# Kernel optimization log

Measured on AMD Instinct MI355X. Metric: run time of the kernel, lower is better.

## Reference

```python
import jax, jax.numpy as jnp
import numpy as np

B, N = 2, 200
IMG = 2048
NC = 4                    # node concepts ('Is*')
NODE_CH = NC * 256        # 1024
EC = 3                    # edge concepts minus 'HigherPri'
AC = 4                    # actions
BBOX_MAX = 1024.0
E = N * (N - 1)

# static fully-connected directed edge list (src=i, dst=j, i!=j), row-major order
_ii, _jj = np.meshgrid(np.arange(N), np.arange(N), indexing='ij')
_m = _ii != _jj
SRC = jnp.asarray(_ii[_m])
DST = jnp.asarray(_jj[_m])


def _lin(k, fin, fout):
    kw, kb = jax.random.split(k)
    s = 1.0 / np.sqrt(fin)
    return (jax.random.uniform(kw, (fin, fout), jnp.float32, -s, s),
            jax.random.uniform(kb, (fout,), jnp.float32, -s, s))


def setup_inputs():
    ks = jax.random.split(jax.random.key(0), 16)
    p = {}
    p['roi_features'] = jax.random.normal(ks[0], (B, N, IMG), jnp.float32)
    p['batch_bboxes'] = jax.random.uniform(ks[1], (B, N, 4), jnp.float32) * BBOX_MAX
    p['batch_directions'] = jax.random.normal(ks[2], (B, N, 4), jnp.float32)
    p['batch_priorities'] = jax.random.normal(ks[3], (B, N), jnp.float32)
    p['w1'], p['b1'] = _lin(ks[4], IMG, 512)
    p['w2'], p['b2'] = _lin(ks[5], 512, 256)
    p['w3'], p['b3'] = _lin(ks[6], 256, NODE_CH)
    p['wi'], p['bi'] = _lin(ks[7], NODE_CH, NC)
    p['we1'], p['be1'] = _lin(ks[8], 16, 256)
    p['we2'], p['be2'] = _lin(ks[9], 256, 64)
    p['we3'], p['be3'] = _lin(ks[10], 64, EC)
    p['wp1'], p['bp1'] = _lin(ks[11], EC + 1, 128)
    p['wp2'], p['bp2'] = _lin(ks[12], 128, NODE_CH * AC)
    p['root_w'], _ = _lin(ks[13], NODE_CH, AC)
    _, p['root_b'] = _lin(ks[14], NODE_CH, AC)
    return p


def reference(roi_features, batch_bboxes, batch_directions, batch_priorities,
              w1, b1, w2, b2, w3, b3, wi, bi,
              we1, be1, we2, be2, we3, be3,
              wp1, bp1, wp2, bp2, root_w, root_b):
    # node concept embedding MLP: [B,N,IMG] -> [B,N,NODE_CH]
    h = jax.nn.relu(roi_features @ w1 + b1)
    h = jax.nn.relu(h @ w2 + b2)
    node_concepts = h @ w3 + b3
    node_concepts_explicit = jax.nn.sigmoid(node_concepts @ wi + bi)

    # pairwise attributes for all directed edges (same ordering as torch masks)
    node_attr = jnp.concatenate([batch_bboxes / BBOX_MAX, batch_directions], -1)  # [B,N,8]
    pair = jnp.concatenate([node_attr[:, SRC], node_attr[:, DST]], -1)            # [B,E,16]
    eh = jax.nn.relu(pair @ we1 + be1)
    eh = jax.nn.relu(eh @ we2 + be2)
    edge_attributes = jax.nn.sigmoid(eh @ we3 + be3)                              # [B,E,EC]
    higher_pri = (batch_priorities[:, SRC] > batch_priorities[:, DST]).astype(jnp.float32)
    edge_attributes = jnp.concatenate([edge_attributes, higher_pri[..., None]], -1)  # [B,E,EC+1]

    # NNConv on graph 0: per-edge weight matrix, gather-matmul-scatter
    x = node_concepts[0]                 # [N, NODE_CH]
    e = edge_attributes[0]               # [E, EC+1]
    w = jax.nn.relu(e @ wp1 + bp1) @ wp2 + bp2
    w = w.reshape(E, NODE_CH, AC)        # [E, NODE_CH, AC]
    msg = jnp.einsum('ei,eio->eo', x[SRC], w)          # [E, AC]
    agg = jax.ops.segment_sum(msg, DST, num_segments=N)  # [N, AC]
    next_actions = agg + x @ root_w + root_b
    return (next_actions, node_concepts_explicit[0], edge_attributes[0])
```

## Files before the change

### kernel.cpp

```cpp
#include <hip/hip_runtime.h>
#include <math.h>

#define NN 200
#define ETOT 39800

typedef float float4v __attribute__((ext_vector_type(4)));
typedef short short8 __attribute__((ext_vector_type(8)));
typedef unsigned int uint4v __attribute__((ext_vector_type(4)));

__device__ __forceinline__ float sigf(float x) { return 1.0f / (1.0f + expf(-x)); }

__device__ __forceinline__ unsigned short f2b(float f) {
  unsigned u = __float_as_uint(f);
  u += 0x7fffu + ((u >> 16) & 1u);
  return (unsigned short)(u >> 16);
}
__device__ __forceinline__ float b2f16(unsigned short u) {
  return __uint_as_float(((unsigned)u) << 16);
}
__device__ __forceinline__ unsigned pkbf(float a, float b) {
  return (unsigned)f2b(a) | ((unsigned)f2b(b) << 16);
}

__global__ __launch_bounds__(256) void k_prep(
    const float* __restrict__ w1, const float* __restrict__ w2, const float* __restrict__ w3,
    const float* __restrict__ wp2, const float* __restrict__ we2,
    const float* __restrict__ bbox, const float* __restrict__ dir,
    const float* __restrict__ we1, const float* __restrict__ be1,
    const float* __restrict__ roi, const float* __restrict__ wp1,
    unsigned short* __restrict__ w1T, unsigned short* __restrict__ w2T,
    unsigned short* __restrict__ w3T, unsigned short* __restrict__ WrT,
    unsigned short* __restrict__ we2T, unsigned short* __restrict__ roiB,
    float* __restrict__ P, float* __restrict__ Q, float* __restrict__ wp1T) {
  __shared__ float lds[64][65];
  const int b = blockIdx.x, tid = threadIdx.x;

  if (b < 352) {
    const float* Wf;
    unsigned short* Wt;
    int K, N, t;
    if (b < 256) { Wf = w1; Wt = w1T; K = 2048; N = 512; t = b; }
    else if (b < 288) { Wf = w2; Wt = w2T; K = 512; N = 256; t = b - 256; }
    else { Wf = w3; Wt = w3T; K = 256; N = 1024; t = b - 288; }
    const int K64 = K >> 6;
    const int kt = t % K64, nt = t / K64;
#pragma unroll 4
    for (int i = 0; i < 16; ++i) {
      int idx = tid + i * 256;
      int r = idx >> 6, c = idx & 63;
      lds[r][c] = Wf[(size_t)(kt * 64 + r) * N + nt * 64 + c];
    }
    __syncthreads();
#pragma unroll 4
    for (int i = 0; i < 16; ++i) {
      int idx = tid + i * 256;
      int r = idx >> 6, c = idx & 63;
      Wt[(size_t)(nt * 64 + r) * K + kt * 64 + c] = f2b(lds[c][r]);
    }
  } else if (b < 480) {
    int k = b - 352;
    int o = tid >> 6, l = tid & 63;
    const float* src = wp2 + (size_t)k * 4096;
    unsigned short* dst = WrT + (size_t)(k * 4 + o) * 1024;
    for (int i = l; i < 1024; i += 64) dst[i] = f2b(src[i * 4 + o]);
  } else if (b < 496) {
    int f = (b - 480) * 256 + tid;
    int c = f >> 6, k0 = (f & 63) * 4;
#pragma unroll
    for (int q = 0; q < 4; ++q)
      we2T[c * 256 + k0 + q] = f2b(we2[(k0 + q) * 64 + c]);
  } else if (b < 696) {
    int n = b - 496, c = tid;
    float a[8];
#pragma unroll
    for (int r = 0; r < 4; ++r) a[r] = bbox[n * 4 + r] * (1.0f / 1024.0f);
#pragma unroll
    for (int r = 0; r < 4; ++r) a[4 + r] = dir[n * 4 + r];
    float p = be1[c], q = 0.0f;
#pragma unroll
    for (int r = 0; r < 8; ++r) {
      p += a[r] * we1[r * 256 + c];
      q += a[r] * we1[(8 + r) * 256 + c];
    }
    P[n * 256 + c] = p;
    Q[n * 256 + c] = q;
  } else if (b < 896) {
    int n = b - 696;
    const float4v* R4 = (const float4v*)(roi + (size_t)n * 2048);
    unsigned long long* O = (unsigned long long*)(roiB + (size_t)n * 2048);
#pragma unroll
    for (int j = 0; j < 2; ++j) {
      int idx = tid + j * 256;
      float4v v = R4[idx];
      union { unsigned short us[4]; unsigned long long ll; } pk;
#pragma unroll
      for (int q = 0; q < 4; ++q) pk.us[q] = f2b(v[q]);
      O[idx] = pk.ll;
    }
  } else {
    if (tid < 128) {
      float4v v = {wp1[tid], wp1[128 + tid], wp1[256 + tid], wp1[384 + tid]};
      ((float4v*)wp1T)[tid] = v;
    }
  }
}

template <int KSTEPS, int RELU, int OUTF32, int HASBIAS>
__global__ __launch_bounds__(256) void gemm_mf(const unsigned short* __restrict__ A,
                                               const unsigned short* __restrict__ B,
                                               const float* __restrict__ bias,
                                               void* __restrict__ Cout, int N) {
  constexpr int K = KSTEPS * 128;
  const int tid = threadIdx.x, lane = tid & 63, wv = tid >> 6;
  const int m0 = blockIdx.x * 16, n0 = blockIdx.y * 16;
  const int mr = lane & 15, quad = lane >> 4;
  const unsigned short* Ap = A + (size_t)(m0 + mr) * K + wv * (KSTEPS * 32) + quad * 8;
  const unsigned short* Bp = B + (size_t)(n0 + mr) * K + wv * (KSTEPS * 32) + quad * 8;
  float4v acc = {0.f, 0.f, 0.f, 0.f};
#pragma unroll
  for (int s = 0; s < KSTEPS; ++s) {
    short8 af = *(const short8*)(Ap + s * 32);
    short8 bf = *(const short8*)(Bp + s * 32);
    acc = __builtin_amdgcn_mfma_f32_16x16x32_bf16(af, bf, acc, 0, 0, 0);
  }
  __shared__ float red[4][16][17];
#pragma unroll
  for (int r = 0; r < 4; ++r) red[wv][quad * 4 + r][mr] = acc[r];
  __syncthreads();
  const int row = tid >> 4, col = tid & 15;
  float v = red[0][row][col] + red[1][row][col] + red[2][row][col] + red[3][row][col];
  if (HASBIAS) v += bias[n0 + col];
  if (RELU) v = fmaxf(v, 0.f);
  if (OUTF32)
    ((float*)Cout)[(size_t)(m0 + row) * N + n0 + col] = v;
  else
    ((unsigned short*)Cout)[(size_t)(m0 + row) * N + n0 + col] = f2b(v);
}

__global__ __launch_bounds__(256) void k_nodevec(const unsigned short* __restrict__ xB,
                                                 const float* __restrict__ wi, const float* __restrict__ bi,
                                                 const float* __restrict__ root_w, const float* __restrict__ root_b,
                                                 const float* __restrict__ bp2,
                                                 float* __restrict__ out_nce, float* __restrict__ U,
                                                 float* __restrict__ out0) {
  const int n = blockIdx.x, tid = threadIdx.x;
  float s[12] = {};
#pragma unroll
  for (int i = 0; i < 4; ++i) {
    int k = tid + i * 256;
    float xv = b2f16(xB[n * 1024 + k]);
    float4v wi4 = ((const float4v*)wi)[k];
    float4v rw4 = ((const float4v*)root_w)[k];
    float4v bp4 = ((const float4v*)bp2)[k];
#pragma unroll
    for (int c = 0; c < 4; ++c) {
      s[c] += xv * wi4[c];
      s[4 + c] += xv * rw4[c];
      s[8 + c] += xv * bp4[c];
    }
  }
  __shared__ float part[4][12];
  const int lane = tid & 63, wv = tid >> 6;
#pragma unroll
  for (int r = 0; r < 12; ++r) {
    float v = s[r];
#pragma unroll
    for (int off = 32; off > 0; off >>= 1) v += __shfl_down(v, off, 64);
    if (lane == 0) part[wv][r] = v;
  }
  __syncthreads();
  if (tid < 12) {
    float v = part[0][tid] + part[1][tid] + part[2][tid] + part[3][tid];
    int kind = tid >> 2, c = tid & 3;
    if (kind == 0) out_nce[n * 4 + c] = sigf(v + bi[c]);
    else if (kind == 1) out0[n * 4 + c] = v + root_b[c];
    else U[n * 4 + c] = v;
  }
}

__global__ __launch_bounds__(256) void k_edge(
    const float* __restrict__ P, const float* __restrict__ Q,
    const unsigned short* __restrict__ we2T,
    const float* __restrict__ be2, const float* __restrict__ we3, const float* __restrict__ be3,
    const float* __restrict__ wp1T, const float* __restrict__ bp1,
    const float* __restrict__ pri,
    const float* __restrict__ T, const float* __restrict__ U,
    float* __restrict__ out0, float* __restrict__ out_ea) {
  __shared__ int src_s[64], dst_s[64];
  __shared__ float ea_s[64][4];
  __shared__ float4v wp1s[128];
  __shared__ float bp1s[128];
  __shared__ float4v Ts[2][128];
  __shared__ float Us[2][4];

  const int tid = threadIdx.x;
  const int e0 = blockIdx.x * 64;
  const int s_lo = e0 / 199;

  if (tid < 64) {
    int e = e0 + tid;
    int i = -1, j = 0;
    if (e < ETOT) {
      i = e / 199;
      int jj = e - i * 199;
      j = jj + (jj >= i ? 1 : 0);
    }
    src_s[tid] = i;
    dst_s[tid] = j;
  }
  if (tid < 128) {
    wp1s[tid] = ((const float4v*)wp1T)[tid];
    bp1s[tid] = bp1[tid];
  }
  {
    int row = tid >> 7, c = tid & 127;
    Ts[row][c] = ((const float4v*)T)[(s_lo + row) * 128 + c];
  }
  if (tid < 8) {
    int s = min(s_lo + (tid >> 2), 199);
    Us[tid >> 2][tid & 3] = U[s * 4 + (tid & 3)];
  }
  __syncthreads();

  const int lane = tid & 63;
  const int wv = tid >> 6;
  const int m = lane & 15;
  const int quad = lane >> 4;
  const int eloc = wv * 16 + m;
  const int si = src_s[eloc];
  const int dj = dst_s[eloc];

  float4v acc[4];
#pragma unroll
  for (int ct = 0; ct < 4; ++ct) { acc[ct][0] = 0.f; acc[ct][1] = 0.f; acc[ct][2] = 0.f; acc[ct][3] = 0.f; }

  const short8* W8 = (const short8*)we2T;

  for (int ks = 0; ks < 8; ++ks) {
    union { short8 s; uint4v u; } af;
    af.s = (short8)0;
    if (si >= 0) {
      const float4v* p4 = (const float4v*)(P + si * 256 + ks * 32 + quad * 8);
      const float4v* q4 = (const float4v*)(Q + dj * 256 + ks * 32 + quad * 8);
      float4v v0 = p4[0] + q4[0];
      float4v v1 = p4[1] + q4[1];
      af.u[0] = pkbf(fmaxf(v0[0], 0.f), fmaxf(v0[1], 0.f));
      af.u[1] = pkbf(fmaxf(v0[2], 0.f), fmaxf(v0[3], 0.f));
      af.u[2] = pkbf(fmaxf(v1[0], 0.f), fmaxf(v1[1], 0.f));
      af.u[3] = pkbf(fmaxf(v1[2], 0.f), fmaxf(v1[3], 0.f));
    }
#pragma unroll
    for (int ct = 0; ct < 4; ++ct) {
      short8 bf = W8[(ct * 16 + m) * 32 + ks * 4 + quad];
      acc[ct] = __builtin_amdgcn_mfma_f32_16x16x32_bf16(af.s, bf, acc[ct], 0, 0, 0);
    }
  }

  float ev[4][3];
#pragma unroll
  for (int r = 0; r < 4; ++r) { ev[r][0] = 0.f; ev[r][1] = 0.f; ev[r][2] = 0.f; }
#pragma unroll
  for (int ct = 0; ct < 4; ++ct) {
    const int col = ct * 16 + m;
    const float b2v = be2[col];
    const float w0 = we3[col * 3 + 0], w1v = we3[col * 3 + 1], w2v = we3[col * 3 + 2];
#pragma unroll
    for (int r = 0; r < 4; ++r) {
      float e2 = fmaxf(acc[ct][r] + b2v, 0.f);
      ev[r][0] += e2 * w0;
      ev[r][1] += e2 * w1v;
      ev[r][2] += e2 * w2v;
    }
  }
#pragma unroll
  for (int r = 0; r < 4; ++r)
#pragma unroll
    for (int p = 0; p < 3; ++p) {
      float v = ev[r][p];
      v += __shfl_xor(v, 1, 64);
      v += __shfl_xor(v, 2, 64);
      v += __shfl_xor(v, 4, 64);
      v += __shfl_xor(v, 8, 64);
      ev[r][p] = v;
    }
  if (m == 0) {
#pragma unroll
    for (int r = 0; r < 4; ++r) {
      int el = wv * 16 + quad * 4 + r;
      int ss = src_s[el], dd = dst_s[el];
      if (ss >= 0) {
        float4v o;
        o[0] = sigf(ev[r][0] + be3[0]);
        o[1] = sigf(ev[r][1] + be3[1]);
        o[2] = sigf(ev[r][2] + be3[2]);
        o[3] = (pri[ss] > pri[dd]) ? 1.0f : 0.0f;
        *(float4v*)&ea_s[el][0] = o;
        *(float4v*)(out_ea + (size_t)(e0 + el) * 4) = o;
      }
    }
  }
  __syncthreads();

  const int ee = tid >> 2, pp = tid & 3;
  const int s2 = src_s[ee], d2 = dst_s[ee];
  float4v pm = {0.f, 0.f, 0.f, 0.f};
  if (s2 >= 0) {
    const int srow = s2 - s_lo;
    const float c0 = ea_s[ee][0], c1 = ea_s[ee][1], c2 = ea_s[ee][2], c3 = ea_s[ee][3];
#pragma unroll 8
    for (int t = pp; t < 128; t += 4) {
      float4v w4 = wp1s[t];
      float hv = bp1s[t] + c0 * w4[0] + c1 * w4[1] + c2 * w4[2] + c3 * w4[3];
      hv = fmaxf(hv, 0.f);
      pm += hv * Ts[srow][t];
    }
  }
#pragma unroll
  for (int o = 0; o < 4; ++o) {
    float v = pm[o];
    v += __shfl_xor(v, 1, 64);
    v += __shfl_xor(v, 2, 64);
    pm[o] = v;
  }
  if (s2 >= 0) atomicAdd(&out0[d2 * 4 + pp], Us[s2 - s_lo][pp] + pm[pp]);
}

extern "C" void kernel_launch(void* const* d_in, const int* in_sizes, int n_in,
                              void* d_out, int out_size, void* d_ws, size_t ws_size,
                              hipStream_t stream) {
  (void)in_sizes; (void)n_in; (void)out_size; (void)ws_size;
  const float* roi   = (const float*)d_in[0];
  const float* bbox  = (const float*)d_in[1];
  const float* dir   = (const float*)d_in[2];
  const float* pri   = (const float*)d_in[3];
  const float* w1    = (const float*)d_in[4];
  const float* b1    = (const float*)d_in[5];
  const float* w2    = (const float*)d_in[6];
  const float* b2    = (const float*)d_in[7];
  const float* w3    = (const float*)d_in[8];
  const float* b3    = (const float*)d_in[9];
  const float* wi    = (const float*)d_in[10];
  const float* bi    = (const float*)d_in[11];
  const float* we1   = (const float*)d_in[12];
  const float* be1   = (const float*)d_in[13];
  const float* we2   = (const float*)d_in[14];
  const float* be2   = (const float*)d_in[15];
  const float* we3   = (const float*)d_in[16];
  const float* be3   = (const float*)d_in[17];
  const float* wp1   = (const float*)d_in[18];
  const float* bp1   = (const float*)d_in[19];
  const float* wp2   = (const float*)d_in[20];
  const float* bp2   = (const float*)d_in[21];
  const float* rootw = (const float*)d_in[22];
  const float* rootb = (const float*)d_in[23];

  float* out0 = (float*)d_out;
  float* out1 = out0 + 800;
  float* out2 = out0 + 1600;

  unsigned short* us = (unsigned short*)d_ws;
  unsigned short* w1T  = us;
  unsigned short* w2T  = us + 1048576;
  unsigned short* w3T  = us + 1179648;
  unsigned short* WrT  = us + 1441792;
  unsigned short* we2T = us + 1966080;
  unsigned short* roiB = us + 1982464;
  unsigned short* h1   = us + 2408448;
  unsigned short* h2   = us + 2514944;
  unsigned short* xB   = us + 2568192;
  float* fb   = (float*)(us + 2781184);
  float* Tm   = fb;
  float* Pm   = fb + 106496;
  float* Qm   = fb + 157696;
  float* Um   = fb + 208896;
  float* wp1T = fb + 209696;

  k_prep<<<897, 256, 0, stream>>>(w1, w2, w3, wp2, we2, bbox, dir, we1, be1, roi, wp1,
                                  w1T, w2T, w3T, WrT, we2T, roiB, Pm, Qm, wp1T);

  gemm_mf<16, 1, 0, 1><<<dim3(13, 32), 256, 0, stream>>>(roiB, w1T, b1, h1, 512);
  gemm_mf<4, 1, 0, 1><<<dim3(13, 16), 256, 0, stream>>>(h1, w2T, b2, h2, 256);
  gemm_mf<2, 0, 0, 1><<<dim3(13, 64), 256, 0, stream>>>(h2, w3T, b3, xB, 1024);

  k_nodevec<<<200, 256, 0, stream>>>(xB, wi, bi, rootw, rootb, bp2, out1, Um, out0);

  gemm_mf<8, 0, 1, 0><<<dim3(13, 32), 256, 0, stream>>>(xB, WrT, nullptr, Tm, 512);

  k_edge<<<622, 256, 0, stream>>>(Pm, Qm, we2T, be2, we3, be3, wp1T, bp1, pri, Tm, Um, out0, out2);
}
```

Baseline: 157.0 us.

## Fold w3 into downstream weights and fuse node-vector GEMM into composed T GEMM

Precomputes a composed weight CT = w3 @ [WrT; wi; root_w; bp2] (plus the b3 bias term) in a GEMM that runs alongside the first MLP layer, so the xB intermediate, the third MLP GEMM and the separate k_nodevec kernel are removed. The T, explicit-concept, root and U outputs now come from one small GEMM on h2 with K=256 instead of K=1024. This cuts kernel launches and the critical-path length. In exchange the weight composition is redone every call and an extra bf16 rounding happens on the composed weights. It also splits MFMA accumulation across two accumulators and uses a hardware packed bf16 convert instruction.

New measurement: 154.4 us (median of 2 runs). No clear change (-1.7%).

```diff
diff --git a/kernel.cpp b/kernel.cpp
--- a/kernel.cpp
+++ b/kernel.cpp
@@ -18,30 +18,32 @@
 __device__ __forceinline__ float b2f16(unsigned short u) {
   return __uint_as_float(((unsigned)u) << 16);
 }
-__device__ __forceinline__ unsigned pkbf(float a, float b) {
-  return (unsigned)f2b(a) | ((unsigned)f2b(b) << 16);
+__device__ __forceinline__ unsigned pk2(float a, float b) {
+  unsigned r;
+  asm("v_cvt_pk_bf16_f32 %0, %1, %2" : "=v"(r) : "v"(a), "v"(b));
+  return r;
 }
 
 __global__ __launch_bounds__(256) void k_prep(
     const float* __restrict__ w1, const float* __restrict__ w2, const float* __restrict__ w3,
-    const float* __restrict__ wp2, const float* __restrict__ we2,
+    const float* __restrict__ b3, const float* __restrict__ wp2, const float* __restrict__ we2,
     const float* __restrict__ bbox, const float* __restrict__ dir,
     const float* __restrict__ we1, const float* __restrict__ be1,
     const float* __restrict__ roi, const float* __restrict__ wp1,
+    const float* __restrict__ wi, const float* __restrict__ rootw, const float* __restrict__ bp2,
     unsigned short* __restrict__ w1T, unsigned short* __restrict__ w2T,
-    unsigned short* __restrict__ w3T, unsigned short* __restrict__ WrT,
+    unsigned short* __restrict__ Ac, unsigned short* __restrict__ Bc,
     unsigned short* __restrict__ we2T, unsigned short* __restrict__ roiB,
     float* __restrict__ P, float* __restrict__ Q, float* __restrict__ wp1T) {
   __shared__ float lds[64][65];
   const int b = blockIdx.x, tid = threadIdx.x;
 
-  if (b < 352) {
+  if (b < 288) {
     const float* Wf;
     unsigned short* Wt;
     int K, N, t;
     if (b < 256) { Wf = w1; Wt = w1T; K = 2048; N = 512; t = b; }
-    else if (b < 288) { Wf = w2; Wt = w2T; K = 512; N = 256; t = b - 256; }
-    else { Wf = w3; Wt = w3T; K = 256; N = 1024; t = b - 288; }
+    else { Wf = w2; Wt = w2T; K = 512; N = 256; t = b - 256; }
     const int K64 = K >> 6;
     const int kt = t % K64, nt = t / K64;
 #pragma unroll 4
@@ -57,20 +59,36 @@
       int r = idx >> 6, c = idx & 63;
       Wt[(size_t)(nt * 64 + r) * K + kt * 64 + c] = f2b(lds[c][r]);
     }
-  } else if (b < 480) {
-    int k = b - 352;
+  } else if (b < 416) {
+    int k = b - 288;
     int o = tid >> 6, l = tid & 63;
     const float* src = wp2 + (size_t)k * 4096;
-    unsigned short* dst = WrT + (size_t)(k * 4 + o) * 1024;
+    unsigned short* dst = Ac + (size_t)(k * 4 + o) * 1024;
     for (int i = l; i < 1024; i += 64) dst[i] = f2b(src[i * 4 + o]);
-  } else if (b < 496) {
-    int f = (b - 480) * 256 + tid;
+  } else if (b < 432) {
+    int r = b - 416;
+    unsigned short* dst = Ac + (size_t)(512 + r) * 1024;
+    const float* src = (r < 4) ? (wi + r) : (r < 8) ? (rootw + (r - 4))
+                     : (r < 12) ? (bp2 + (r - 8)) : nullptr;
+    for (int i = tid; i < 1024; i += 256)
+      dst[i] = src ? f2b(src[i * 4]) : (unsigned short)0;
+  } else if (b < 500) {
+    int rb = (b - 432) * 4;
+#pragma unroll
+    for (int j = 0; j < 16; ++j) {
+      int idx = tid + j * 256;
+      int row = rb + (idx >> 10), i = idx & 1023;
+      float val = (row < 256) ? w3[(size_t)row * 1024 + i] : (row == 256 ? b3[i] : 0.0f);
+      Bc[(size_t)row * 1024 + i] = f2b(val);
+    }
+  } else if (b < 516) {
+    int f = (b - 500) * 256 + tid;
     int c = f >> 6, k0 = (f & 63) * 4;
 #pragma unroll
     for (int q = 0; q < 4; ++q)
       we2T[c * 256 + k0 + q] = f2b(we2[(k0 + q) * 64 + c]);
-  } else if (b < 696) {
-    int n = b - 496, c = tid;
+  } else if (b < 716) {
+    int n = b - 516, c = tid;
     float a[8];
 #pragma unroll
     for (int r = 0; r < 4; ++r) a[r] = bbox[n * 4 + r] * (1.0f / 1024.0f);
@@ -84,17 +102,17 @@
     }
     P[n * 256 + c] = p;
     Q[n * 256 + c] = q;
-  } else if (b < 896) {
-    int n = b - 696;
+  } else if (b < 916) {
+    int n = b - 716;
     const float4v* R4 = (const float4v*)(roi + (size_t)n * 2048);
     unsigned long long* O = (unsigned long long*)(roiB + (size_t)n * 2048);
 #pragma unroll
     for (int j = 0; j < 2; ++j) {
       int idx = tid + j * 256;
       float4v v = R4[idx];
-      union { unsigned short us[4]; unsigned long long ll; } pk;
-#pragma unroll
-      for (int q = 0; q < 4; ++q) pk.us[q] = f2b(v[q]);
+      union { unsigned u[2]; unsigned long long ll; } pk;
+      pk.u[0] = pk2(v[0], v[1]);
+      pk.u[1] = pk2(v[2], v[3]);
       O[idx] = pk.ll;
     }
   } else {
@@ -105,76 +123,91 @@
   }
 }
 
-template <int KSTEPS, int RELU, int OUTF32, int HASBIAS>
-__global__ __launch_bounds__(256) void gemm_mf(const unsigned short* __restrict__ A,
-                                               const unsigned short* __restrict__ B,
-                                               const float* __restrict__ bias,
-                                               void* __restrict__ Cout, int N) {
-  constexpr int K = KSTEPS * 128;
+__device__ __forceinline__ float4v mfma16(short8 a, short8 b, float4v c) {
+  return __builtin_amdgcn_mfma_f32_16x16x32_bf16(a, b, c, 0, 0, 0);
+}
+
+template <int KSTEPS>
+__device__ __forceinline__ float tile_core(const unsigned short* __restrict__ A,
+                                           const unsigned short* __restrict__ B,
+                                           int m0, int n0, int K,
+                                           float (&red)[4][16][17]) {
   const int tid = threadIdx.x, lane = tid & 63, wv = tid >> 6;
-  const int m0 = blockIdx.x * 16, n0 = blockIdx.y * 16;
   const int mr = lane & 15, quad = lane >> 4;
   const unsigned short* Ap = A + (size_t)(m0 + mr) * K + wv * (KSTEPS * 32) + quad * 8;
   const unsigned short* Bp = B + (size_t)(n0 + mr) * K + wv * (KSTEPS * 32) + quad * 8;
-  float4v acc = {0.f, 0.f, 0.f, 0.f};
-#pragma unroll
-  for (int s = 0; s < KSTEPS; ++s) {
-    short8 af = *(const short8*)(Ap + s * 32);
-    short8 bf = *(const short8*)(Bp + s * 32);
-    acc = __builtin_amdgcn_mfma_f32_16x16x32_bf16(af, bf, acc, 0, 0, 0);
-  }
-  __shared__ float red[4][16][17];
+  float4v acc0 = {0.f, 0.f, 0.f, 0.f}, acc1 = {0.f, 0.f, 0.f, 0.f};
+#pragma unroll
+  for (int s = 0; s < KSTEPS; s += 2) {
+    acc0 = mfma16(*(const short8*)(Ap + s * 32), *(const short8*)(Bp + s * 32), acc0);
+    acc1 = mfma16(*(const short8*)(Ap + (s + 1) * 32), *(const short8*)(Bp + (s + 1) * 32), acc1);
+  }
+  float4v acc = acc0 + acc1;
 #pragma unroll
   for (int r = 0; r < 4; ++r) red[wv][quad * 4 + r][mr] = acc[r];
   __syncthreads();
   const int row = tid >> 4, col = tid & 15;
-  float v = red[0][row][col] + red[1][row][col] + red[2][row][col] + red[3][row][col];
-  if (HASBIAS) v += bias[n0 + col];
-  if (RELU) v = fmaxf(v, 0.f);
-  if (OUTF32)
-    ((float*)Cout)[(size_t)(m0 + row) * N + n0 + col] = v;
-  else
-    ((unsigned short*)Cout)[(size_t)(m0 + row) * N + n0 + col] = f2b(v);
-}
-
-__global__ __launch_bounds__(256) void k_nodevec(const unsigned short* __restrict__ xB,
-                                                 const float* __restrict__ wi, const float* __restrict__ bi,
-                                                 const float* __restrict__ root_w, const float* __restrict__ root_b,
-                                                 const float* __restrict__ bp2,
-                                                 float* __restrict__ out_nce, float* __restrict__ U,
-                                                 float* __restrict__ out0) {
-  const int n = blockIdx.x, tid = threadIdx.x;
-  float s[12] = {};
-#pragma unroll
-  for (int i = 0; i < 4; ++i) {
-    int k = tid + i * 256;
-    float xv = b2f16(xB[n * 1024 + k]);
-    float4v wi4 = ((const float4v*)wi)[k];
-    float4v rw4 = ((const float4v*)root_w)[k];
-    float4v bp4 = ((const float4v*)bp2)[k];
-#pragma unroll
-    for (int c = 0; c < 4; ++c) {
-      s[c] += xv * wi4[c];
-      s[4 + c] += xv * rw4[c];
-      s[8 + c] += xv * bp4[c];
-    }
-  }
-  __shared__ float part[4][12];
-  const int lane = tid & 63, wv = tid >> 6;
-#pragma unroll
-  for (int r = 0; r < 12; ++r) {
-    float v = s[r];
-#pragma unroll
-    for (int off = 32; off > 0; off >>= 1) v += __shfl_down(v, off, 64);
-    if (lane == 0) part[wv][r] = v;
-  }
-  __syncthreads();
-  if (tid < 12) {
-    float v = part[0][tid] + part[1][tid] + part[2][tid] + part[3][tid];
-    int kind = tid >> 2, c = tid & 3;
-    if (kind == 0) out_nce[n * 4 + c] = sigf(v + bi[c]);
-    else if (kind == 1) out0[n * 4 + c] = v + root_b[c];
-    else U[n * 4 + c] = v;
+  return red[0][row][col] + red[1][row][col] + red[2][row][col] + red[3][row][col];
+}
+
+__global__ __launch_bounds__(256) void k_gemm1_compose(
+    const unsigned short* __restrict__ roiB, const unsigned short* __restrict__ w1T,
+    const float* __restrict__ b1, unsigned short* __restrict__ h1,
+    const unsigned short* __restrict__ Ac, const unsigned short* __restrict__ Bc,
+    unsigned short* __restrict__ CT, float* __restrict__ biasT) {
+  __shared__ float red[4][16][17];
+  const int bid = blockIdx.x, tid = threadIdx.x;
+  if (bid < 416) {
+    const int m0 = (bid % 13) * 16, n0 = (bid / 13) * 16;
+    float v = tile_core<16>(roiB, w1T, m0, n0, 2048, red);
+    const int row = tid >> 4, col = tid & 15;
+    v += b1[n0 + col];
+    v = fmaxf(v, 0.f);
+    h1[(size_t)(m0 + row) * 512 + n0 + col] = f2b(v);
+  } else {
+    const int t = bid - 416;
+    const int m0 = (t % 33) * 16, n0 = (t / 33) * 16;
+    float v = tile_core<8>(Ac, Bc, m0, n0, 1024, red);
+    const int row = tid >> 4, col = tid & 15;
+    const int c = n0 + col;
+    if (c < 256) CT[(size_t)(m0 + row) * 256 + c] = f2b(v);
+    else if (c == 256) biasT[m0 + row] = v;
+  }
+}
+
+__global__ __launch_bounds__(256) void k_gemm2(const unsigned short* __restrict__ h1,
+                                               const unsigned short* __restrict__ w2T,
+                                               const float* __restrict__ b2,
+                                               unsigned short* __restrict__ h2) {
+  __shared__ float red[4][16][17];
+  const int m0 = blockIdx.x * 16, n0 = blockIdx.y * 16, tid = threadIdx.x;
+  float v = tile_core<4>(h1, w2T, m0, n0, 512, red);
+  const int row = tid >> 4, col = tid & 15;
+  v += b2[n0 + col];
+  v = fmaxf(v, 0.f);
+  h2[(size_t)(m0 + row) * 256 + n0 + col] = f2b(v);
+}
+
+__global__ __launch_bounds__(256) void k_tfused(const unsigned short* __restrict__ h2,
+                                                const unsigned short* __restrict__ CT,
+                                                const float* __restrict__ biasT,
+                                                const float* __restrict__ bi,
+                                                const float* __restrict__ rootb,
+                                                float* __restrict__ Tm, float* __restrict__ out1,
+                                                float* __restrict__ out0, float* __restrict__ U) {
+  __shared__ float red[4][16][17];
+  const int m0 = blockIdx.x * 16, n0 = blockIdx.y * 16, tid = threadIdx.x;
+  float v = tile_core<2>(h2, CT, m0, n0, 256, red);
+  const int row = tid >> 4, col = tid & 15;
+  const int n = m0 + row, c = n0 + col;
+  v += biasT[c];
+  if (c < 512) {
+    Tm[(size_t)n * 512 + c] = v;
+  } else if (n < NN) {
+    int r = c - 512;
+    if (r < 4) out1[n * 4 + r] = sigf(v + bi[r]);
+    else if (r < 8) out0[n * 4 + (r - 4)] = v + rootb[r - 4];
+    else if (r < 12) U[n * 4 + (r - 8)] = v;
   }
 }
 
@@ -244,10 +277,10 @@
       const float4v* q4 = (const float4v*)(Q + dj * 256 + ks * 32 + quad * 8);
       float4v v0 = p4[0] + q4[0];
       float4v v1 = p4[1] + q4[1];
-      af.u[0] = pkbf(fmaxf(v0[0], 0.f), fmaxf(v0[1], 0.f));
-      af.u[1] = pkbf(fmaxf(v0[2], 0.f), fmaxf(v0[3], 0.f));
-      af.u[2] = pkbf(fmaxf(v1[0], 0.f), fmaxf(v1[1], 0.f));
-      af.u[3] = pkbf(fmaxf(v1[2], 0.f), fmaxf(v1[3], 0.f));
+      af.u[0] = pk2(fmaxf(v0[0], 0.f), fmaxf(v0[1], 0.f));
+      af.u[1] = pk2(fmaxf(v0[2], 0.f), fmaxf(v0[3], 0.f));
+      af.u[2] = pk2(fmaxf(v1[0], 0.f), fmaxf(v1[1], 0.f));
+      af.u[3] = pk2(fmaxf(v1[2], 0.f), fmaxf(v1[3], 0.f));
     }
 #pragma unroll
     for (int ct = 0; ct < 4; ++ct) {
@@ -361,30 +394,30 @@
   unsigned short* us = (unsigned short*)d_ws;
   unsigned short* w1T  = us;
   unsigned short* w2T  = us + 1048576;
-  unsigned short* w3T  = us + 1179648;
-  unsigned short* WrT  = us + 1441792;
-  unsigned short* we2T = us + 1966080;
-  unsigned short* roiB = us + 1982464;
-  unsigned short* h1   = us + 2408448;
-  unsigned short* h2   = us + 2514944;
-  unsigned short* xB   = us + 2568192;
-  float* fb   = (float*)(us + 2781184);
-  float* Tm   = fb;
-  float* Pm   = fb + 106496;
-  float* Qm   = fb + 157696;
-  float* Um   = fb + 208896;
-  float* wp1T = fb + 209696;
-
-  k_prep<<<897, 256, 0, stream>>>(w1, w2, w3, wp2, we2, bbox, dir, we1, be1, roi, wp1,
-                                  w1T, w2T, w3T, WrT, we2T, roiB, Pm, Qm, wp1T);
-
-  gemm_mf<16, 1, 0, 1><<<dim3(13, 32), 256, 0, stream>>>(roiB, w1T, b1, h1, 512);
-  gemm_mf<4, 1, 0, 1><<<dim3(13, 16), 256, 0, stream>>>(h1, w2T, b2, h2, 256);
-  gemm_mf<2, 0, 0, 1><<<dim3(13, 64), 256, 0, stream>>>(h2, w3T, b3, xB, 1024);
-
-  k_nodevec<<<200, 256, 0, stream>>>(xB, wi, bi, rootw, rootb, bp2, out1, Um, out0);
-
-  gemm_mf<8, 0, 1, 0><<<dim3(13, 32), 256, 0, stream>>>(xB, WrT, nullptr, Tm, 512);
-
-  k_edge<<<622, 256, 0, stream>>>(Pm, Qm, we2T, be2, we3, be3, wp1T, bp1, pri, Tm, Um, out0, out2);
-}
+  unsigned short* Ac   = us + 1179648;
+  unsigned short* Bc   = us + 1720320;
+  unsigned short* we2T = us + 1998848;
+  unsigned short* roiB = us + 2015232;
+  unsigned short* h1   = us + 2441216;
+  unsigned short* h2   = us + 2547712;
+  unsigned short* CT   = us + 2600960;
+  float* fb    = (float*)(us + 2736128);
+  float* Tm    = fb;
+  float* Pm    = fb + 106496;
+  float* Qm    = fb + 157696;
+  float* Um    = fb + 208896;
+  float* wp1Tp = fb + 209696;
+  float* biasT = fb + 210208;
+
+  k_prep<<<917, 256, 0, stream>>>(w1, w2, w3, b3, wp2, we2, bbox, dir, we1, be1, roi, wp1,
+                                  wi, rootw, bp2,
+                                  w1T, w2T, Ac, Bc, we2T, roiB, Pm, Qm, wp1Tp);
+
+  k_gemm1_compose<<<977, 256, 0, stream>>>(roiB, w1T, b1, h1, Ac, Bc, CT, biasT);
+
+  k_gemm2<<<dim3(13, 16), 256, 0, stream>>>(h1, w2T, b2, h2);
+
+  k_tfused<<<dim3(13, 33), 256, 0, stream>>>(h2, CT, biasT, bi, rootb, Tm, out1, out0, Um);
+
+  k_edge<<<622, 256, 0, stream>>>(Pm, Qm, we2T, be2, we3, be3, wp1Tp, bp1, pri, Tm, Um, out0, out2);
+}
```
